# Kernel optimization log

Measured on AMD Instinct MI355X. Metric: run time of the kernel, lower is better.

## Reference

```python
import jax, jax.numpy as jnp
import numpy as np

B, CLN, QL, IH, IW = 64, 32, 32, 16, 16
CDF, SL = 256, 128
IDF = CLN * IH * IW  # 8192


def setup_inputs() -> dict:
    key = jax.random.key(0)
    k1, k2, k3 = jax.random.split(key, 3)
    inp = jax.random.normal(k1, (B, CLN, QL, IH, IW), dtype=jnp.float32)
    context = jax.random.normal(k2, (B, CDF, SL), dtype=jnp.float32)
    # Conv2d(cdf, idf, 1, bias=False) weight, squeezed to [idf, cdf]
    W = jax.random.normal(k3, (IDF, CDF), dtype=jnp.float32) * (1.0 / np.sqrt(CDF))
    return {"input": inp, "context": context, "W": W}


def reference(input, context, W):
    b, cln, queryL, ih, iw = input.shape
    idf = cln * ih * iw
    sourceL = context.shape[2]
    # target: b x queryL x (cln*ih*iw)
    targetT = jnp.transpose(input, (0, 2, 1, 3, 4)).reshape(b, queryL, idf)
    # 1x1 conv projection of context: b x idf x sourceL
    sourceT = jnp.einsum('oc,bcs->bos', W, context)
    # attention scores and softmax over sourceL (nn.Softmax on 2D -> dim=1)
    attn = jnp.einsum('bqd,bds->bqs', targetT, sourceT)  # b x queryL x sourceL
    attn = jax.nn.softmax(attn, axis=-1)
    attnT = jnp.transpose(attn, (0, 2, 1))  # b x sourceL x queryL
    # weighted context: b x idf x queryL
    wc = jnp.einsum('bds,bsq->bdq', sourceT, attnT)
    # faithful to torch .view: raw row-major reinterpretation of [b, idf, queryL]
    wc = wc.reshape(b, queryL, cln, ih, iw)
    wc = jnp.transpose(wc, (0, 2, 1, 3, 4))  # b x cln x queryL x ih x iw
    return (wc, attnT)
```

## Files before the change

kernel.cpp:

```cpp
#include <hip/hip_runtime.h>
#include <math.h>


#define ZK 16

typedef _Float16 f16x8 __attribute__((ext_vector_type(8)));
typedef float f32x4 __attribute__((ext_vector_type(4)));

__global__ __launch_bounds__(256) void k0a_prep(const float* __restrict__ Wm,
                                                _Float16* __restrict__ Wth,
                                                _Float16* __restrict__ Wtl) {
    const int kb = blockIdx.x;
    const int t = threadIdx.x;
    __shared__ float tile[32][260];
    {
        const int r = t >> 3;
        const int c0 = (t & 7) * 32;
        const float* src = Wm + (long)(kb * 32 + r) * 256 + c0;
#pragma unroll
        for (int i = 0; i < 8; ++i) {
            float4 v = *(const float4*)(src + i * 4);
            tile[r][c0 + i * 4 + 0] = v.x;
            tile[r][c0 + i * 4 + 1] = v.y;
            tile[r][c0 + i * 4 + 2] = v.z;
            tile[r][c0 + i * 4 + 3] = v.w;
        }
    }
    __syncthreads();
    const int lane = t & 63;
    const int quad = lane >> 4, l15 = lane & 15;
#pragma unroll
    for (int i = 0; i < 4; ++i) {
        int nsub = (t >> 6) * 4 + i;
        f16x8 oh, ol;
#pragma unroll
        for (int j = 0; j < 8; ++j) {
            float f = tile[quad * 8 + j][nsub * 16 + l15];
            _Float16 h = (_Float16)f;
            oh[j] = h;
            ol[j] = (_Float16)(f - (float)h);
        }
        long addr = ((long)(kb * 16 + nsub) * 64 + lane) * 8;
        *(f16x8*)(Wth + addr) = oh;
        *(f16x8*)(Wtl + addr) = ol;
    }
}

__global__ __launch_bounds__(256) void k0b_prep(const float* __restrict__ Wm,
                                                _Float16* __restrict__ Wbf) {
    const int t = threadIdx.x;
    const int fid = blockIdx.x * 4 + (t >> 6);
    const int mb = fid >> 3, kb4 = fid & 7;
    const int lane = t & 63;
    const int quad = lane >> 4, l15 = lane & 15;
    const float* src = Wm + (long)(mb * 16 + l15) * 256 + kb4 * 32 + quad * 8;
    float4 u0 = *(const float4*)(src);
    float4 u1 = *(const float4*)(src + 4);
    f16x8 o;
    o[0] = (_Float16)u0.x; o[1] = (_Float16)u0.y;
    o[2] = (_Float16)u0.z; o[3] = (_Float16)u0.w;
    o[4] = (_Float16)u1.x; o[5] = (_Float16)u1.y;
    o[6] = (_Float16)u1.z; o[7] = (_Float16)u1.w;
    *(f16x8*)(Wbf + ((long)fid * 64 + lane) * 8) = o;
}

__global__ __launch_bounds__(512, 2) void k1_mfma(const float* __restrict__ inp,
                                                  const _Float16* __restrict__ Wth,
                                                  const _Float16* __restrict__ Wtl,
                                                  float* __restrict__ tWpart) {
    const int m0 = blockIdx.x * 128;
    const int kz = blockIdx.y;
    const int t = threadIdx.x;
    const int lane = t & 63, wv = t >> 6;
    const int quad = lane >> 4, l15 = lane & 15;
    const int mi = wv >> 2;
    const int ni = wv & 3;

    const float* arow0;
    const float* arow1;
    const float* arow2;
    const float* arow3;
    {
        int mA = m0 + (mi * 4 + 0) * 16 + l15;
        arow0 = inp + (long)(mA >> 5) * 262144 + (long)(mA & 31) * 256;
        mA = m0 + (mi * 4 + 1) * 16 + l15;
        arow1 = inp + (long)(mA >> 5) * 262144 + (long)(mA & 31) * 256;
        mA = m0 + (mi * 4 + 2) * 16 + l15;
        arow2 = inp + (long)(mA >> 5) * 262144 + (long)(mA & 31) * 256;
        mA = m0 + (mi * 4 + 3) * 16 + l15;
        arow3 = inp + (long)(mA >> 5) * 262144 + (long)(mA & 31) * 256;
    }

    f32x4 acc[4][4];
#pragma unroll
    for (int i = 0; i < 4; ++i)
#pragma unroll
        for (int j = 0; j < 4; ++j) acc[i][j] = (f32x4){0.f, 0.f, 0.f, 0.f};

    float4 Ar[2][4][2];
    f16x8 Bh[2][4], Bl[2][4];

    {
        const int k0g = kz * 512;
        const long off = (long)(k0g >> 8) * 8192 + (k0g & 255) + quad * 8;
        Ar[0][0][0] = *(const float4*)(arow0 + off); Ar[0][0][1] = *(const float4*)(arow0 + off + 4);
        Ar[0][1][0] = *(const float4*)(arow1 + off); Ar[0][1][1] = *(const float4*)(arow1 + off + 4);
        Ar[0][2][0] = *(const float4*)(arow2 + off); Ar[0][2][1] = *(const float4*)(arow2 + off + 4);
        Ar[0][3][0] = *(const float4*)(arow3 + off); Ar[0][3][1] = *(const float4*)(arow3 + off + 4);
        const long base = ((long)((kz * 16) * 16 + ni * 4) * 64 + lane) * 8;
#pragma unroll
        for (int j = 0; j < 4; ++j) {
            Bh[0][j] = *(const f16x8*)(Wth + base + (long)j * 512);
            Bl[0][j] = *(const f16x8*)(Wtl + base + (long)j * 512);
        }
    }

#pragma unroll
    for (int it = 0; it < 16; ++it) {
        const int cur = it & 1, nxt = cur ^ 1;
        if (it < 15) {
            const int k0g = kz * 512 + (it + 1) * 32;
            const long off = (long)(k0g >> 8) * 8192 + (k0g & 255) + quad * 8;
            Ar[nxt][0][0] = *(const float4*)(arow0 + off); Ar[nxt][0][1] = *(const float4*)(arow0 + off + 4);
            Ar[nxt][1][0] = *(const float4*)(arow1 + off); Ar[nxt][1][1] = *(const float4*)(arow1 + off + 4);
            Ar[nxt][2][0] = *(const float4*)(arow2 + off); Ar[nxt][2][1] = *(const float4*)(arow2 + off + 4);
            Ar[nxt][3][0] = *(const float4*)(arow3 + off); Ar[nxt][3][1] = *(const float4*)(arow3 + off + 4);
            const long base = ((long)((kz * 16 + it + 1) * 16 + ni * 4) * 64 + lane) * 8;
#pragma unroll
            for (int j = 0; j < 4; ++j) {
                Bh[nxt][j] = *(const f16x8*)(Wth + base + (long)j * 512);
                Bl[nxt][j] = *(const f16x8*)(Wtl + base + (long)j * 512);
            }
        }
        f16x8 ah[4], al[4];
#pragma unroll
        for (int i = 0; i < 4; ++i) {
            float ff[8] = {Ar[cur][i][0].x, Ar[cur][i][0].y, Ar[cur][i][0].z, Ar[cur][i][0].w,
                           Ar[cur][i][1].x, Ar[cur][i][1].y, Ar[cur][i][1].z, Ar[cur][i][1].w};
#pragma unroll
            for (int j = 0; j < 8; ++j) {
                _Float16 h = (_Float16)ff[j];
                ah[i][j] = h;
                al[i][j] = (_Float16)(ff[j] - (float)h);
            }
        }
#pragma unroll
        for (int i = 0; i < 4; ++i)
#pragma unroll
            for (int j = 0; j < 4; ++j) {
                acc[i][j] = __builtin_amdgcn_mfma_f32_16x16x32_f16(ah[i], Bh[cur][j], acc[i][j], 0, 0, 0);
                acc[i][j] = __builtin_amdgcn_mfma_f32_16x16x32_f16(al[i], Bh[cur][j], acc[i][j], 0, 0, 0);
                acc[i][j] = __builtin_amdgcn_mfma_f32_16x16x32_f16(ah[i], Bl[cur][j], acc[i][j], 0, 0, 0);
            }
    }

    float* outp = tWpart + (long)kz * 524288;
#pragma unroll
    for (int i = 0; i < 4; ++i) {
        const int mbase = m0 + (mi * 4 + i) * 16 + quad * 4;
#pragma unroll
        for (int j = 0; j < 4; ++j) {
            const int c = (ni * 4 + j) * 16 + l15;
#pragma unroll
            for (int rg = 0; rg < 4; ++rg)
                outp[(long)(mbase + rg) * 256 + c] = acc[i][j][rg];
        }
    }
}

__global__ __launch_bounds__(256) void k2_logits_softmax(const float* __restrict__ tWpart,
                                                         const float* __restrict__ ctx,
                                                         float* __restrict__ attnT) {
    const int qg = blockIdx.x;
    const int b  = blockIdx.y;
    const int t  = threadIdx.x;
    __shared__ float tw4[4][256];
#pragma unroll
    for (int qq = 0; qq < 4; ++qq) {
        const float* p = tWpart + (long)(b * 32 + qg * 4 + qq) * 256 + t;
        float s = 0.f;
#pragma unroll
        for (int z = 0; z < ZK; ++z) s += p[(long)z * 524288];
        tw4[qq][t] = s;
    }
    __syncthreads();
    const int q = t >> 6, lane = t & 63;
    const float* ctxb = ctx + (long)b * 32768 + lane * 2;
    float ax = 0.f, ay = 0.f;
#pragma unroll 4
    for (int c = 0; c < 256; ++c) {
        float tw = tw4[q][c];
        float2 cv = *(const float2*)(ctxb + c * 128);
        ax = fmaf(tw, cv.x, ax);
        ay = fmaf(tw, cv.y, ay);
    }
    float mx = fmaxf(ax, ay);
#pragma unroll
    for (int m = 1; m <= 32; m <<= 1) mx = fmaxf(mx, __shfl_xor(mx, m));
    float ex = expf(ax - mx);
    float ey = expf(ay - mx);
    float sm = ex + ey;
#pragma unroll
    for (int m = 1; m <= 32; m <<= 1) sm += __shfl_xor(sm, m);
    float inv = 1.f / sm;
    ex *= inv; ey *= inv;
    float* o = attnT + (long)b * 4096 + (qg * 4 + q);
    o[(lane * 2 + 0) * 32] = ex;
    o[(lane * 2 + 1) * 32] = ey;
}

__global__ __launch_bounds__(256) void k3_ctxA(const float* __restrict__ ctx,
                                               const float* __restrict__ attnT,
                                               _Float16* __restrict__ ctxAqf) {
    const int cg = blockIdx.x;
    const int b  = blockIdx.y;
    const int t  = threadIdx.x;
    __shared__ float at[128][32];
    __shared__ float cs[32][132];
#pragma unroll
    for (int i = 0; i < 4; ++i)
        *(float4*)((float*)at + i * 1024 + t * 4) =
            *(const float4*)(attnT + (long)b * 4096 + i * 1024 + t * 4);
#pragma unroll
    for (int i = 0; i < 4; ++i) {
        int idx = i * 256 + t;
        int c = idx >> 5, sseg = (idx & 31) * 4;
        *(float4*)&cs[c][sseg] = *(const float4*)(ctx + (long)b * 32768 + (long)(cg * 32 + c) * 128 + sseg);
    }
    __syncthreads();
    const int c = t >> 3;
    const int qs = (t & 7) * 4;
    float4 acc = make_float4(0.f, 0.f, 0.f, 0.f);
#pragma unroll 4
    for (int s = 0; s < 128; ++s) {
        float cv = cs[c][s];
        float4 av = *(const float4*)&at[s][qs];
        acc.x = fmaf(cv, av.x, acc.x);
        acc.y = fmaf(cv, av.y, acc.y);
        acc.z = fmaf(cv, av.z, acc.z);
        acc.w = fmaf(cv, av.w, acc.w);
    }
    const int cglob = cg * 32 + c;
    const long cpart = (long)(cglob >> 5) * 64 + 16 * ((cglob >> 3) & 3);
    float vals[4] = {acc.x, acc.y, acc.z, acc.w};
#pragma unroll
    for (int u = 0; u < 4; ++u) {
        int n = b * 32 + qs + u;
        long addr = ((long)(n >> 4) * 8 * 64 + cpart + (n & 15)) * 8 + (cglob & 7);
        ctxAqf[addr] = (_Float16)vals[u];
    }
}

__global__ __launch_bounds__(256) void k4_mfma(const _Float16* __restrict__ Wbf,
                                               const _Float16* __restrict__ ctxAqf,
                                               float* __restrict__ out0) {
    const int t = threadIdx.x;
    const int lane = t & 63, wv = t >> 6;
    const int mb = blockIdx.x * 4 + wv;
    const int nb0 = blockIdx.y * 8;
    const _Float16* abase = Wbf + ((long)mb * 8 * 64 + lane) * 8;
    const _Float16* bbase = ctxAqf + ((long)nb0 * 8 * 64 + lane) * 8;

    f32x4 acc[8];
#pragma unroll
    for (int j = 0; j < 8; ++j) acc[j] = (f32x4){0.f, 0.f, 0.f, 0.f};

#pragma unroll
    for (int kb = 0; kb < 8; ++kb) {
        f16x8 af = *(const f16x8*)(abase + (long)kb * 512);
#pragma unroll
        for (int j = 0; j < 8; ++j) {
            f16x8 bf = *(const f16x8*)(bbase + (long)(j * 8 + kb) * 512);
            acc[j] = __builtin_amdgcn_mfma_f32_16x16x32_f16(af, bf, acc[j], 0, 0, 0);
        }
    }
    const int quad = lane >> 4, col = lane & 15;
#pragma unroll
    for (int j = 0; j < 8; ++j) {
        const int n = (nb0 + j) * 16 + col;
        float* ob = out0 + (long)(n >> 5) * 262144 + (n & 31);
#pragma unroll
        for (int rg = 0; rg < 4; ++rg) {
            const int d = mb * 16 + quad * 4 + rg;
            ob[(long)((d >> 3) & 31) * 8192 + (long)(d >> 8) * 256 + (long)(d & 7) * 32] = acc[j][rg];
        }
    }
}

extern "C" void kernel_launch(void* const* d_in, const int* in_sizes, int n_in,
                              void* d_out, int out_size, void* d_ws, size_t ws_size,
                              hipStream_t stream) {
    const float* inp = (const float*)d_in[0];
    const float* ctx = (const float*)d_in[1];
    const float* Wm  = (const float*)d_in[2];
    float* out0 = (float*)d_out;
    float* out1 = out0 + 16777216;

    float* wsf = (float*)d_ws;
    float* tWpart = wsf;
    _Float16* Wbf    = (_Float16*)wsf;
    _Float16* ctxAqf = (_Float16*)(wsf + 1048576);
    _Float16* Wth = (_Float16*)(wsf + 8388608);
    _Float16* Wtl = Wth + 2097152;

    hipLaunchKernelGGL(k0a_prep, dim3(256), dim3(256), 0, stream, Wm, Wth, Wtl);
    hipLaunchKernelGGL(k1_mfma, dim3(16, ZK), dim3(512), 0, stream, inp, Wth, Wtl, tWpart);
    hipLaunchKernelGGL(k2_logits_softmax, dim3(8, 64), dim3(256), 0, stream, tWpart, ctx, out1);
    hipLaunchKernelGGL(k0b_prep, dim3(1024), dim3(256), 0, stream, Wm, Wbf);
    hipLaunchKernelGGL(k3_ctxA, dim3(8, 64), dim3(256), 0, stream, ctx, out1, ctxAqf);
    hipLaunchKernelGGL(k4_mfma, dim3(128, 16), dim3(256), 0, stream, Wbf, ctxAqf, out0);
}
```

Baseline: 231.8 us.

## Stage A tiles through LDS with direct global-to-LDS loads and swizzle

The fp32 input tile in the split-fp16 MFMA GEMM is now loaded cooperatively into a double-buffered shared-memory tile with global_load_lds, using an XOR swizzle. Previously each wave loaded its own A rows from global memory straight into registers. Each element is now fetched once per block instead of once per wave column, which cuts redundant global traffic and register use. In exchange it adds explicit vmcnt/lgkmcnt waits and two block barriers per k-iteration, which may serialize the pipeline.

```diff
diff --git a/kernel.cpp b/kernel.cpp
--- a/kernel.cpp
+++ b/kernel.cpp
@@ -6,6 +6,11 @@
 
 typedef _Float16 f16x8 __attribute__((ext_vector_type(8)));
 typedef float f32x4 __attribute__((ext_vector_type(4)));
+
+#define GLDS16(gp, lp)                                                          \
+    __builtin_amdgcn_global_load_lds(                                           \
+        (const __attribute__((address_space(1))) void*)(gp),                    \
+        (__attribute__((address_space(3))) void*)(lp), 16, 0, 0)
 
 __global__ __launch_bounds__(256) void k0a_prep(const float* __restrict__ Wm,
                                                 _Float16* __restrict__ Wth,
@@ -76,20 +81,22 @@
     const int mi = wv >> 2;
     const int ni = wv & 3;
 
-    const float* arow0;
-    const float* arow1;
-    const float* arow2;
-    const float* arow3;
+    __shared__ float As[2][128][32];
+
+    const int srow = t >> 3;
+    const int swc = ((t & 7) ^ (srow & 7)) * 4;
+    const float* sb0;
+    const float* sb1;
     {
-        int mA = m0 + (mi * 4 + 0) * 16 + l15;
-        arow0 = inp + (long)(mA >> 5) * 262144 + (long)(mA & 31) * 256;
-        mA = m0 + (mi * 4 + 1) * 16 + l15;
-        arow1 = inp + (long)(mA >> 5) * 262144 + (long)(mA & 31) * 256;
-        mA = m0 + (mi * 4 + 2) * 16 + l15;
-        arow2 = inp + (long)(mA >> 5) * 262144 + (long)(mA & 31) * 256;
-        mA = m0 + (mi * 4 + 3) * 16 + l15;
-        arow3 = inp + (long)(mA >> 5) * 262144 + (long)(mA & 31) * 256;
-    }
+        int mA = m0 + srow;
+        sb0 = inp + (long)(mA >> 5) * 262144 + (long)(mA & 31) * 256 + swc;
+        mA = m0 + 64 + srow;
+        sb1 = inp + (long)(mA >> 5) * 262144 + (long)(mA & 31) * 256 + swc;
+    }
+    float* lbase0 = &As[0][0][0] + wv * 256;
+    float* lbase1 = &As[0][64][0] + wv * 256;
+    float* lbase0b = &As[1][0][0] + wv * 256;
+    float* lbase1b = &As[1][64][0] + wv * 256;
 
     f32x4 acc[4][4];
 #pragma unroll
@@ -97,21 +104,18 @@
 #pragma unroll
         for (int j = 0; j < 4; ++j) acc[i][j] = (f32x4){0.f, 0.f, 0.f, 0.f};
 
-    float4 Ar[2][4][2];
     f16x8 Bh[2][4], Bl[2][4];
 
     {
         const int k0g = kz * 512;
-        const long off = (long)(k0g >> 8) * 8192 + (k0g & 255) + quad * 8;
-        Ar[0][0][0] = *(const float4*)(arow0 + off); Ar[0][0][1] = *(const float4*)(arow0 + off + 4);
-        Ar[0][1][0] = *(const float4*)(arow1 + off); Ar[0][1][1] = *(const float4*)(arow1 + off + 4);
-        Ar[0][2][0] = *(const float4*)(arow2 + off); Ar[0][2][1] = *(const float4*)(arow2 + off + 4);
-        Ar[0][3][0] = *(const float4*)(arow3 + off); Ar[0][3][1] = *(const float4*)(arow3 + off + 4);
-        const long base = ((long)((kz * 16) * 16 + ni * 4) * 64 + lane) * 8;
+        const long o = (long)(k0g >> 8) * 8192 + (k0g & 255);
+        GLDS16(sb0 + o, lbase0);
+        GLDS16(sb1 + o, lbase1);
+        const long bb = ((long)((kz * 16) * 16 + ni * 4) * 64 + lane) * 8;
 #pragma unroll
         for (int j = 0; j < 4; ++j) {
-            Bh[0][j] = *(const f16x8*)(Wth + base + (long)j * 512);
-            Bl[0][j] = *(const f16x8*)(Wtl + base + (long)j * 512);
+            Bh[0][j] = *(const f16x8*)(Wth + bb + (long)j * 512);
+            Bl[0][j] = *(const f16x8*)(Wtl + bb + (long)j * 512);
         }
     }
 
@@ -120,23 +124,30 @@
         const int cur = it & 1, nxt = cur ^ 1;
         if (it < 15) {
             const int k0g = kz * 512 + (it + 1) * 32;
-            const long off = (long)(k0g >> 8) * 8192 + (k0g & 255) + quad * 8;
-            Ar[nxt][0][0] = *(const float4*)(arow0 + off); Ar[nxt][0][1] = *(const float4*)(arow0 + off + 4);
-            Ar[nxt][1][0] = *(const float4*)(arow1 + off); Ar[nxt][1][1] = *(const float4*)(arow1 + off + 4);
-            Ar[nxt][2][0] = *(const float4*)(arow2 + off); Ar[nxt][2][1] = *(const float4*)(arow2 + off + 4);
-            Ar[nxt][3][0] = *(const float4*)(arow3 + off); Ar[nxt][3][1] = *(const float4*)(arow3 + off + 4);
-            const long base = ((long)((kz * 16 + it + 1) * 16 + ni * 4) * 64 + lane) * 8;
+            const long o = (long)(k0g >> 8) * 8192 + (k0g & 255);
+            if (nxt) { GLDS16(sb0 + o, lbase0b); GLDS16(sb1 + o, lbase1b); }
+            else     { GLDS16(sb0 + o, lbase0);  GLDS16(sb1 + o, lbase1);  }
+            const long bb = ((long)((kz * 16 + it + 1) * 16 + ni * 4) * 64 + lane) * 8;
 #pragma unroll
             for (int j = 0; j < 4; ++j) {
-                Bh[nxt][j] = *(const f16x8*)(Wth + base + (long)j * 512);
-                Bl[nxt][j] = *(const f16x8*)(Wtl + base + (long)j * 512);
+                Bh[nxt][j] = *(const f16x8*)(Wth + bb + (long)j * 512);
+                Bl[nxt][j] = *(const f16x8*)(Wtl + bb + (long)j * 512);
             }
         }
+        __builtin_amdgcn_sched_barrier(0);
+        if (it < 15) asm volatile("s_waitcnt vmcnt(10)" ::: "memory");
+        else         asm volatile("s_waitcnt vmcnt(0)" ::: "memory");
+        __builtin_amdgcn_sched_barrier(0);
+        __builtin_amdgcn_s_barrier();
+
         f16x8 ah[4], al[4];
 #pragma unroll
         for (int i = 0; i < 4; ++i) {
-            float ff[8] = {Ar[cur][i][0].x, Ar[cur][i][0].y, Ar[cur][i][0].z, Ar[cur][i][0].w,
-                           Ar[cur][i][1].x, Ar[cur][i][1].y, Ar[cur][i][1].z, Ar[cur][i][1].w};
+            const int row = (mi * 4 + i) * 16 + l15;
+            const int x = row & 7;
+            float4 f0 = *(const float4*)&As[cur][row][((quad * 2) ^ x) * 4];
+            float4 f1 = *(const float4*)&As[cur][row][((quad * 2 + 1) ^ x) * 4];
+            float ff[8] = {f0.x, f0.y, f0.z, f0.w, f1.x, f1.y, f1.z, f1.w};
 #pragma unroll
             for (int j = 0; j < 8; ++j) {
                 _Float16 h = (_Float16)ff[j];
@@ -144,6 +155,10 @@
                 al[i][j] = (_Float16)(ff[j] - (float)h);
             }
         }
+        asm volatile("s_waitcnt lgkmcnt(0)" ::: "memory");
+        __builtin_amdgcn_sched_barrier(0);
+        __builtin_amdgcn_s_barrier();
+
 #pragma unroll
         for (int i = 0; i < 4; ++i)
 #pragma unroll
```

Result: faster. 219.6 us (-5.3%).
